# Kernel tuning notes

Measured on AMD Instinct MI355X. Metric: run time of the kernel, lower is better.

## Reference

```python
import jax, jax.numpy as jnp
import numpy as np

EMBED_DIM = 1024
NUM_HEADS = 16
HEAD_DIM = EMBED_DIM // NUM_HEADS
SCALE = HEAD_DIM ** -0.5


def setup_inputs() -> dict:
    key = jax.random.key(0)
    k1, k2, k3, k4 = jax.random.split(key, 4)
    B, N, D = 2, 2048, EMBED_DIM
    x = jax.random.normal(k1, (B, N, D), dtype=jnp.float32)
    # nn.Linear weights stored as [out, in]; we keep [in, out] for x @ W
    w_qkv = jax.random.normal(k2, (D, 3 * D), dtype=jnp.float32) * (D ** -0.5)
    w_proj = jax.random.normal(k3, (D, D), dtype=jnp.float32) * (D ** -0.5)
    b_proj = jax.random.normal(k4, (D,), dtype=jnp.float32) * 0.01
    return {"x": x, "w_qkv": w_qkv, "w_proj": w_proj, "b_proj": b_proj}


def reference(x, w_qkv, w_proj, b_proj):
    B, N, D = x.shape
    H, Hd = NUM_HEADS, HEAD_DIM
    qkv = x @ w_qkv  # [B, N, 3D]
    q, k, v = jnp.split(qkv, 3, axis=-1)
    # [B, N, D] -> [B, H, N, Hd]
    split_heads = lambda t: t.reshape(B, N, H, Hd).transpose(0, 2, 1, 3)
    q, k, v = split_heads(q), split_heads(k), split_heads(v)
    a = jnp.einsum("bhqd,bhkd->bhqk", q, k) * SCALE
    a = jax.nn.softmax(a, axis=-1)
    out = jnp.einsum("bhqk,bhkd->bhqd", a, v)
    out = out.transpose(0, 2, 1, 3).reshape(B, N, D)
    return out @ w_proj + b_proj
```

## Files before the change

kernel.cpp:

```cpp
#include <hip/hip_runtime.h>
#include <stdint.h>

typedef __attribute__((ext_vector_type(8))) short bf16x8;
typedef __attribute__((ext_vector_type(4))) float f32x4;
typedef __attribute__((ext_vector_type(4))) float float4v;
typedef __attribute__((ext_vector_type(8))) unsigned short u16x8;

#define DEV __device__ __forceinline__

DEV unsigned short f2bf(float f) {
    union { float f; uint32_t u; } v; v.f = f;
    uint32_t u = v.u;
    return (unsigned short)((u + 0x7FFFu + ((u >> 16) & 1u)) >> 16);
}

DEV unsigned int cvt_pk_bf16(float lo, float hi) {
    unsigned int r;
    asm("v_cvt_pk_bf16_f32 %0, %1, %2" : "=v"(r) : "v"(lo), "v"(hi));
    return r;
}

#if __has_builtin(__builtin_amdgcn_global_load_lds)
#define HAVE_GLDS 1
typedef const unsigned char __attribute__((address_space(1)))* as1p;
typedef unsigned char __attribute__((address_space(3)))* as3p;
DEV void gload16(const unsigned short* g, unsigned short* l) {
    __builtin_amdgcn_global_load_lds((as1p)(const void*)g, (as3p)(void*)l, 16, 0, 0);
}
#else
#define HAVE_GLDS 0
#endif

__global__ void k_cvt_all(const float* __restrict__ x, unsigned short* __restrict__ xb,
                          const float* __restrict__ wqkv, unsigned short* __restrict__ wqkvT,
                          const float* __restrict__ wproj, unsigned short* __restrict__ wprojT) {
    __shared__ alignas(16) unsigned short tile[64][65];
    const int blk = blockIdx.x;
    const int t = threadIdx.x;
    if (blk < 4096) {
        const int i = blk * 256 + t;
        float4v v = *(const float4v*)(x + (size_t)i * 4);
        union { unsigned short s[4]; uint64_t q; } o;
        o.s[0] = f2bf(v[0]); o.s[1] = f2bf(v[1]); o.s[2] = f2bf(v[2]); o.s[3] = f2bf(v[3]);
        *(uint64_t*)(xb + (size_t)i * 4) = o.q;
        return;
    }
    const float* w; unsigned short* wt; int R, C, bx, by;
    if (blk < 4864) {
        const int b2 = blk - 4096;
        w = wqkv; wt = wqkvT; R = 1024; C = 3072;
        bx = b2 % 48; by = b2 / 48;
    } else {
        const int b3 = blk - 4864;
        w = wproj; wt = wprojT; R = 1024; C = 1024;
        bx = b3 % 16; by = b3 / 16;
    }
    const int tr = by * 64, tc = bx * 64;
#pragma unroll
    for (int p = 0; p < 4; ++p) {
        int r = p * 16 + (t >> 4);
        int c = (t & 15) * 4;
        float4v v = *(const float4v*)(w + (size_t)(tr + r) * C + tc + c);
#pragma unroll
        for (int j = 0; j < 4; ++j) tile[r][c + j] = f2bf(v[j]);
    }
    __syncthreads();
#pragma unroll
    for (int p = 0; p < 2; ++p) {
        int r2 = p * 32 + (t >> 3);
        int k0 = (t & 7) * 8;
        u16x8 o;
#pragma unroll
        for (int j = 0; j < 8; ++j) o[j] = tile[k0 + j][r2];
        *(u16x8*)(wt + (size_t)(tc + r2) * R + tr + k0) = o;
    }
}

template <int OUT_BF16, int BM, int BN, int NTY>
__global__ __launch_bounds__(256)
void k_gemm_bt(const unsigned short* __restrict__ A,
               const unsigned short* __restrict__ Bt,
               void* __restrict__ Cp, const float* __restrict__ bias,
               unsigned short* __restrict__ vt_out,
               int M, int N, int K) {
    constexpr int MFR = BM / 32;
    constexpr int NFR = BN / 32;
    __shared__ alignas(16) unsigned short lA[BM * 64];
    __shared__ alignas(16) unsigned short lB[BN * 64];
    const int t = threadIdx.x;
    const int w = t >> 6, l = t & 63;
    const int l15 = l & 15, l4 = l >> 4;
    const int wm = (w >> 1) * (BM / 2), wn = (w & 1) * (BN / 2);

    const int cpx = gridDim.x >> 3;
    const int wk = (blockIdx.x & 7) * cpx + (blockIdx.x >> 3);
    const int bx = wk / NTY, by = wk % NTY;
    const size_t bm = (size_t)by * BM, bn = (size_t)bx * BN;

    int offA[MFR][2], offB[NFR][2];
#pragma unroll
    for (int f = 0; f < MFR; ++f) {
        const int ra = wm + f * 16 + l15;
#pragma unroll
        for (int kc = 0; kc < 2; ++kc)
            offA[f][kc] = ra * 64 + (((kc * 4 + l4) ^ (ra & 7)) << 3);
    }
#pragma unroll
    for (int f = 0; f < NFR; ++f) {
        const int rb = wn + f * 16 + l15;
#pragma unroll
        for (int kc = 0; kc < 2; ++kc)
            offB[f][kc] = rb * 64 + (((kc * 4 + l4) ^ (rb & 7)) << 3);
    }

#if HAVE_GLDS
    const int srow8 = l >> 3;
    const int scol  = (l & 7) ^ srow8;
    const unsigned short* gA = A  + (bm + w * (BM / 4) + srow8) * (size_t)K + scol * 8;
    const unsigned short* gB = Bt + (bn + w * (BN / 4) + srow8) * (size_t)K + scol * 8;
    unsigned short* dA = lA + (w * (BM / 4)) * 64;
    unsigned short* dB = lB + (w * (BN / 4)) * 64;
#else
    const int srow = t >> 3, sslot = t & 7;
    const int swoff = srow * 64 + ((sslot ^ (srow & 7)) << 3);
    const unsigned short* pA = A + (bm + srow) * (size_t)K + sslot * 8;
    const unsigned short* pB = Bt + (bn + srow) * (size_t)K + sslot * 8;
#endif

    const f32x4 zf = {0.f, 0.f, 0.f, 0.f};
    f32x4 acc[MFR][NFR];
#pragma unroll
    for (int i = 0; i < MFR; ++i)
#pragma unroll
        for (int j = 0; j < NFR; ++j) acc[i][j] = zf;

    for (int kt = 0; kt < K; kt += 64) {
#if HAVE_GLDS
        __syncthreads();
#pragma unroll
        for (int i = 0; i < BM / 32; ++i)
            gload16(gA + (size_t)i * 8 * K + kt, dA + i * 8 * 64);
#pragma unroll
        for (int i = 0; i < BN / 32; ++i)
            gload16(gB + (size_t)i * 8 * K + kt, dB + i * 8 * 64);
        __syncthreads();
#else
        bf16x8 ra[BM / 32], rb[BN / 32];
#pragma unroll
        for (int p = 0; p < BM / 32; ++p)
            ra[p] = *(const bf16x8*)(pA + (size_t)p * 32 * K + kt);
#pragma unroll
        for (int p = 0; p < BN / 32; ++p)
            rb[p] = *(const bf16x8*)(pB + (size_t)p * 32 * K + kt);
        __syncthreads();
#pragma unroll
        for (int p = 0; p < BM / 32; ++p)
            *(bf16x8*)(lA + p * 32 * 64 + swoff) = ra[p];
#pragma unroll
        for (int p = 0; p < BN / 32; ++p)
            *(bf16x8*)(lB + p * 32 * 64 + swoff) = rb[p];
        __syncthreads();
#endif
#pragma unroll
        for (int kc = 0; kc < 2; ++kc) {
            bf16x8 af[MFR], bfr[NFR];
#pragma unroll
            for (int f = 0; f < MFR; ++f) af[f] = *(const bf16x8*)(lA + offA[f][kc]);
#pragma unroll
            for (int f = 0; f < NFR; ++f) bfr[f] = *(const bf16x8*)(lB + offB[f][kc]);
#pragma unroll
            for (int mf = 0; mf < MFR; ++mf)
#pragma unroll
                for (int nf = 0; nf < NFR; ++nf)
                    acc[mf][nf] = __builtin_amdgcn_mfma_f32_16x16x32_bf16(
                        af[mf], bfr[nf], acc[mf][nf], 0, 0, 0);
        }
    }

    if (OUT_BF16) {
        unsigned short* C = (unsigned short*)Cp;
#pragma unroll
        for (int nf = 0; nf < NFR; ++nf) {
            const int col0 = (int)bn + wn + nf * 16;
            if (vt_out && col0 >= 2048) {
                const int bb = (int)(bm >> 11);
                const int n0 = (int)(bm & 2047) + wm + l4 * 4;
                const int d = col0 - 2048 + l15;
                unsigned short* vrow = vt_out + ((size_t)(bb * 16 + (d >> 6)) * 64 + (d & 63)) * 2048;
#pragma unroll
                for (int mf = 0; mf < MFR; ++mf) {
                    union { unsigned short s[4]; uint64_t q; } u;
#pragma unroll
                    for (int j = 0; j < 4; ++j) u.s[j] = f2bf(acc[mf][nf][j]);
                    *(uint64_t*)(vrow + n0 + mf * 16) = u.q;
                }
            } else {
                const size_t col = (size_t)col0 + l15;
#pragma unroll
                for (int mf = 0; mf < MFR; ++mf) {
                    const size_t row = bm + wm + mf * 16 + l4 * 4;
#pragma unroll
                    for (int j = 0; j < 4; ++j)
                        C[(row + j) * (size_t)N + col] = f2bf(acc[mf][nf][j]);
                }
            }
        }
    } else {
        float* C = (float*)Cp;
#pragma unroll
        for (int nf = 0; nf < NFR; ++nf) {
            const size_t col = bn + wn + nf * 16 + l15;
            const float bv = bias[col];
#pragma unroll
            for (int mf = 0; mf < MFR; ++mf) {
                const size_t row = bm + wm + mf * 16 + l4 * 4;
#pragma unroll
                for (int j = 0; j < 4; ++j)
                    C[(row + j) * (size_t)N + col] = acc[mf][nf][j] + bv;
            }
        }
    }
}

__global__ __launch_bounds__(512, 2)
void k_attn(const unsigned short* __restrict__ qkv, const unsigned short* __restrict__ vt,
            unsigned short* __restrict__ attn_out) {
    __shared__ alignas(16) unsigned short lK[2][64 * 64];
    __shared__ alignas(16) unsigned short lV[2][64 * 64];
    __shared__ alignas(16) unsigned short lP[8][16 * 64];
    const int t = threadIdx.x, w = t >> 6, l = t & 63;
    const int l15 = l & 15, l4 = l >> 4;
    const int wk = (blockIdx.x & 7) * 64 + (blockIdx.x >> 3);
    const int bh = wk >> 4, b = bh >> 4, h = bh & 15;
    const int qb = (wk & 15) * 128;
    const float QSCALE = 0.18033688011112042f;
    const float M_FIX = 10.0f;

    const unsigned short* qptr =
        qkv + (size_t)(b * 2048 + qb + w * 16 + l15) * 3072 + h * 64 + l4 * 8;
    const bf16x8 aq0 = *(const bf16x8*)(qptr);
    const bf16x8 aq1 = *(const bf16x8*)(qptr + 32);

    const int srow = t >> 3, sslot = t & 7;
    const int swoff = srow * 64 + ((sslot ^ (srow & 7)) << 3);
    const unsigned short* kptr = qkv + (size_t)(b * 2048 + srow) * 3072 + 1024 + h * 64 + sslot * 8;
    const unsigned short* vptr = vt + (size_t)(bh * 64 + srow) * 2048 + sslot * 8;

    int offK[4][2];
#pragma unroll
    for (int nf = 0; nf < 4; ++nf) {
        const int r = nf * 16 + l15;
#pragma unroll
        for (int kc = 0; kc < 2; ++kc)
            offK[nf][kc] = r * 64 + (((kc * 4 + l4) ^ (r & 7)) << 3);
    }
    int offPw[4];
#pragma unroll
    for (int nf = 0; nf < 4; ++nf) {
        const int c = nf * 16 + l4 * 4;
        offPw[nf] = l15 * 64 + (((c >> 3) ^ (l15 & 7)) << 3) + (c & 7);
    }

    const f32x4 zf = {0.f, 0.f, 0.f, 0.f};
    f32x4 o[4];
#pragma unroll
    for (int df = 0; df < 4; ++df) o[df] = zf;
    f32x4 accl = zf;
    unsigned short* Pw = &lP[w][0];
    const bf16x8 ones8 = {(short)0x3F80, (short)0x3F80, (short)0x3F80, (short)0x3F80,
                          (short)0x3F80, (short)0x3F80, (short)0x3F80, (short)0x3F80};

    {
        const bf16x8 rk = *(const bf16x8*)(kptr);
        const bf16x8 rv = *(const bf16x8*)(vptr);
        *(bf16x8*)(&lK[0][0] + swoff) = rk;
        *(bf16x8*)(&lV[0][0] + swoff) = rv;
        __syncthreads();
    }

#pragma unroll 2
    for (int kt = 0; kt < 2048; kt += 64) {
        const int cur = (kt >> 6) & 1;
        const unsigned short* K = &lK[cur][0];
        const unsigned short* V = &lV[cur][0];

        bf16x8 rk, rv;
        const bool more = (kt + 64) < 2048;
        if (more) {
            rk = *(const bf16x8*)(kptr + (size_t)(kt + 64) * 3072);
            rv = *(const bf16x8*)(vptr + kt + 64);
        }

        f32x4 s[4];
        __builtin_amdgcn_s_setprio(1);
#pragma unroll
        for (int nf = 0; nf < 4; ++nf) {
            const bf16x8 kf0 = *(const bf16x8*)(K + offK[nf][0]);
            const bf16x8 kf1 = *(const bf16x8*)(K + offK[nf][1]);
            f32x4 a = zf;
            a = __builtin_amdgcn_mfma_f32_16x16x32_bf16(kf0, aq0, a, 0, 0, 0);
            a = __builtin_amdgcn_mfma_f32_16x16x32_bf16(kf1, aq1, a, 0, 0, 0);
            s[nf] = a;
        }
        __builtin_amdgcn_s_setprio(0);

#pragma unroll
        for (int nf = 0; nf < 4; ++nf) {
            const float p0 = exp2f(fmaf(s[nf][0], QSCALE, -M_FIX));
            const float p1 = exp2f(fmaf(s[nf][1], QSCALE, -M_FIX));
            const float p2 = exp2f(fmaf(s[nf][2], QSCALE, -M_FIX));
            const float p3 = exp2f(fmaf(s[nf][3], QSCALE, -M_FIX));
            union { unsigned int d[2]; uint64_t q; } u;
            u.d[0] = cvt_pk_bf16(p0, p1);
            u.d[1] = cvt_pk_bf16(p2, p3);
            *(uint64_t*)(Pw + offPw[nf]) = u.q;
        }

        const bf16x8 ap0 = *(const bf16x8*)(Pw + l15 * 64 + ((l4 ^ (l15 & 7)) << 3));
        const bf16x8 ap1 = *(const bf16x8*)(Pw + l15 * 64 + (((4 + l4) ^ (l15 & 7)) << 3));
        __builtin_amdgcn_s_setprio(1);
        accl = __builtin_amdgcn_mfma_f32_16x16x32_bf16(ap0, ones8, accl, 0, 0, 0);
        accl = __builtin_amdgcn_mfma_f32_16x16x32_bf16(ap1, ones8, accl, 0, 0, 0);
#pragma unroll
        for (int df = 0; df < 4; ++df) {
            const int r = df * 16 + l15;
            const bf16x8 bv0 = *(const bf16x8*)(V + r * 64 + ((l4 ^ (r & 7)) << 3));
            const bf16x8 bv1 = *(const bf16x8*)(V + r * 64 + (((4 + l4) ^ (r & 7)) << 3));
            o[df] = __builtin_amdgcn_mfma_f32_16x16x32_bf16(ap0, bv0, o[df], 0, 0, 0);
            o[df] = __builtin_amdgcn_mfma_f32_16x16x32_bf16(ap1, bv1, o[df], 0, 0, 0);
        }
        __builtin_amdgcn_s_setprio(0);

        if (more) {
            *(bf16x8*)(&lK[cur ^ 1][0] + swoff) = rk;
            *(bf16x8*)(&lV[cur ^ 1][0] + swoff) = rv;
        }
        __syncthreads();
    }

    const float r0 = 1.0f / accl[0];
    const float r1 = 1.0f / accl[1];
    const float r2 = 1.0f / accl[2];
    const float r3 = 1.0f / accl[3];
    const int rowb = b * 2048 + qb + w * 16 + l4 * 4;
#pragma unroll
    for (int df = 0; df < 4; ++df) {
        const int d = df * 16 + l15;
        attn_out[(size_t)(rowb + 0) * 1024 + h * 64 + d] = f2bf(o[df][0] * r0);
        attn_out[(size_t)(rowb + 1) * 1024 + h * 64 + d] = f2bf(o[df][1] * r1);
        attn_out[(size_t)(rowb + 2) * 1024 + h * 64 + d] = f2bf(o[df][2] * r2);
        attn_out[(size_t)(rowb + 3) * 1024 + h * 64 + d] = f2bf(o[df][3] * r3);
    }
}

extern "C" void kernel_launch(void* const* d_in, const int* in_sizes, int n_in,
                              void* d_out, int out_size, void* d_ws, size_t ws_size,
                              hipStream_t stream) {
    const float* x      = (const float*)d_in[0];
    const float* w_qkv  = (const float*)d_in[1];
    const float* w_proj = (const float*)d_in[2];
    const float* b_proj = (const float*)d_in[3];
    float* out = (float*)d_out;

    char* ws = (char*)d_ws;
    unsigned short* xb     = (unsigned short*)(ws + 0);
    unsigned short* wqkvT  = (unsigned short*)(ws + 8388608);
    unsigned short* wprojT = (unsigned short*)(ws + 14680064);
    unsigned short* qkv    = (unsigned short*)(ws + 16777216);
    unsigned short* vt     = (unsigned short*)(ws + 41943040);
    unsigned short* attn   = (unsigned short*)(ws + 50331648);

    k_cvt_all<<<dim3(5120), dim3(256), 0, stream>>>(x, xb, w_qkv, wqkvT, w_proj, wprojT);
    k_gemm_bt<1, 128, 96, 32><<<dim3(1024), dim3(256), 0, stream>>>(
        xb, wqkvT, (void*)qkv, (const float*)nullptr, vt, 4096, 3072, 1024);
    k_attn<<<dim3(512), dim3(512), 0, stream>>>(qkv, vt, attn);
    k_gemm_bt<0, 64, 64, 64><<<dim3(1024), dim3(256), 0, stream>>>(
        attn, wprojT, (void*)out, b_proj, (unsigned short*)nullptr, 4096, 1024, 1024);
}
```

Baseline: 119.1 us.

## Double attention block size to 256 queries so more waves share each K/V tile

The attention kernel now uses 1024-thread blocks covering 256 query rows per (batch, head), instead of 512 threads covering 128 rows. The grid is halved and the block-to-work mapping is adjusted. The first 512 threads stage K and the other 512 stage V, so each thread issues one global load per tile instead of two. This halves the global K/V traffic per query and the per-thread load work, at the cost of more waves waiting at each barrier and a different occupancy profile with fewer blocks.

```diff
diff --git a/kernel.cpp b/kernel.cpp
--- a/kernel.cpp
+++ b/kernel.cpp
@@ -222,17 +222,17 @@
     }
 }
 
-__global__ __launch_bounds__(512, 2)
+__global__ __launch_bounds__(1024, 1)
 void k_attn(const unsigned short* __restrict__ qkv, const unsigned short* __restrict__ vt,
             unsigned short* __restrict__ attn_out) {
     __shared__ alignas(16) unsigned short lK[2][64 * 64];
     __shared__ alignas(16) unsigned short lV[2][64 * 64];
-    __shared__ alignas(16) unsigned short lP[8][16 * 64];
+    __shared__ alignas(16) unsigned short lP[16][16 * 64];
     const int t = threadIdx.x, w = t >> 6, l = t & 63;
     const int l15 = l & 15, l4 = l >> 4;
-    const int wk = (blockIdx.x & 7) * 64 + (blockIdx.x >> 3);
-    const int bh = wk >> 4, b = bh >> 4, h = bh & 15;
-    const int qb = (wk & 15) * 128;
+    const int wk = (blockIdx.x & 7) * 32 + (blockIdx.x >> 3);
+    const int bh = wk >> 3, b = bh >> 4, h = bh & 15;
+    const int qb = (wk & 7) * 256;
     const float QSCALE = 0.18033688011112042f;
     const float M_FIX = 10.0f;
 
@@ -241,10 +241,16 @@
     const bf16x8 aq0 = *(const bf16x8*)(qptr);
     const bf16x8 aq1 = *(const bf16x8*)(qptr + 32);
 
-    const int srow = t >> 3, sslot = t & 7;
+    const int st = t & 511;
+    const int srow = st >> 3, sslot = st & 7;
     const int swoff = srow * 64 + ((sslot ^ (srow & 7)) << 3);
-    const unsigned short* kptr = qkv + (size_t)(b * 2048 + srow) * 3072 + 1024 + h * 64 + sslot * 8;
-    const unsigned short* vptr = vt + (size_t)(bh * 64 + srow) * 2048 + sslot * 8;
+    const bool isK = t < 512;
+    const unsigned short* sptr = isK
+        ? qkv + (size_t)(b * 2048 + srow) * 3072 + 1024 + h * 64 + sslot * 8
+        : vt + (size_t)(bh * 64 + srow) * 2048 + sslot * 8;
+    const int sstride = isK ? 3072 : 1;
+    unsigned short* sdst0 = isK ? &lK[0][0] : &lV[0][0];
+    unsigned short* sdst1 = isK ? &lK[1][0] : &lV[1][0];
 
     int offK[4][2];
 #pragma unroll
@@ -271,10 +277,8 @@
                           (short)0x3F80, (short)0x3F80, (short)0x3F80, (short)0x3F80};
 
     {
-        const bf16x8 rk = *(const bf16x8*)(kptr);
-        const bf16x8 rv = *(const bf16x8*)(vptr);
-        *(bf16x8*)(&lK[0][0] + swoff) = rk;
-        *(bf16x8*)(&lV[0][0] + swoff) = rv;
+        const bf16x8 r0 = *(const bf16x8*)(sptr);
+        *(bf16x8*)(sdst0 + swoff) = r0;
         __syncthreads();
     }
 
@@ -284,12 +288,10 @@
         const unsigned short* K = &lK[cur][0];
         const unsigned short* V = &lV[cur][0];
 
-        bf16x8 rk, rv;
+        bf16x8 rs;
         const bool more = (kt + 64) < 2048;
-        if (more) {
-            rk = *(const bf16x8*)(kptr + (size_t)(kt + 64) * 3072);
-            rv = *(const bf16x8*)(vptr + kt + 64);
-        }
+        if (more)
+            rs = *(const bf16x8*)(sptr + (size_t)(kt + 64) * sstride);
 
         f32x4 s[4];
         __builtin_amdgcn_s_setprio(1);
@@ -331,10 +333,8 @@
         }
         __builtin_amdgcn_s_setprio(0);
 
-        if (more) {
-            *(bf16x8*)(&lK[cur ^ 1][0] + swoff) = rk;
-            *(bf16x8*)(&lV[cur ^ 1][0] + swoff) = rv;
-        }
+        if (more)
+            *(bf16x8*)((cur ? sdst0 : sdst1) + swoff) = rs;
         __syncthreads();
     }
 
@@ -373,7 +373,7 @@
     k_cvt_all<<<dim3(5120), dim3(256), 0, stream>>>(x, xb, w_qkv, wqkvT, w_proj, wprojT);
     k_gemm_bt<1, 128, 96, 32><<<dim3(1024), dim3(256), 0, stream>>>(
         xb, wqkvT, (void*)qkv, (const float*)nullptr, vt, 4096, 3072, 1024);
-    k_attn<<<dim3(512), dim3(512), 0, stream>>>(qkv, vt, attn);
+    k_attn<<<dim3(256), dim3(1024), 0, stream>>>(qkv, vt, attn);
     k_gemm_bt<0, 64, 64, 64><<<dim3(1024), dim3(256), 0, stream>>>(
         attn, wprojT, (void*)out, b_proj, (unsigned short*)nullptr, 4096, 1024, 1024);
 }
```

New measurement: 117.3 us. No clear change (-1.6%).
